# Optimization experiments

Measured on AMD Instinct MI355X. Metric: run time of the kernel, lower is better.

## Reference

```python
import jax, jax.numpy as jnp
import numpy as np

D_MODEL = 768
N_HEADS = 12
D_K = D_MODEL // N_HEADS
BATCH = 1
SEQ = 4096


def setup_inputs() -> dict:
    key = jax.random.key(0)
    kx, kq, kk, kv, ko = jax.random.split(key, 5)
    s = 1.0 / np.sqrt(D_MODEL)
    return {
        "x": jax.random.normal(kx, (BATCH, SEQ, D_MODEL), dtype=jnp.float32),
        "wq": jax.random.normal(kq, (D_MODEL, D_MODEL), dtype=jnp.float32) * s,
        "wk": jax.random.normal(kk, (D_MODEL, D_MODEL), dtype=jnp.float32) * s,
        "wv": jax.random.normal(kv, (D_MODEL, D_MODEL), dtype=jnp.float32) * s,
        "wo": jax.random.normal(ko, (D_MODEL, D_MODEL), dtype=jnp.float32) * s,
    }


def reference(x, wq, wk, wv, wo):
    B, S, D = x.shape
    H, dk = N_HEADS, D_K
    # nn.Linear(x) = x @ W.T ; reshape to [B,H,S,dk]
    def proj(w):
        return (x @ w.T).reshape(B, S, H, dk).transpose(0, 2, 1, 3)
    q, k, v = proj(wq), proj(wk), proj(wv)
    scores = jnp.einsum('bhqd,bhkd->bhqk', q, k) / np.sqrt(dk).astype(np.float32)
    attn = jax.nn.softmax(scores, axis=-1)
    out = jnp.einsum('bhqk,bhkd->bhqd', attn, v)
    out = out.transpose(0, 2, 1, 3).reshape(B, S, D)
    return out @ wo.T
```

## Files before the change

### kernel.cpp

```cpp
#include <hip/hip_runtime.h>
#include <stdint.h>

#define SEQ 4096
#define DMODEL 768
#define NHEADS 12
#define DKH 64

typedef __attribute__((ext_vector_type(8))) short short8;
typedef __attribute__((ext_vector_type(4))) float floatx4;
typedef __attribute__((ext_vector_type(16))) float floatx16;

__device__ __forceinline__ unsigned short f2bf(float f) {
    unsigned int u = __float_as_uint(f);
    u += 0x7fffu + ((u >> 16) & 1u);
    return (unsigned short)(u >> 16);
}

__device__ __forceinline__ float exp2fast(float x) {
    return __builtin_amdgcn_exp2f(x);
}

__device__ __forceinline__ unsigned int cvt_pk_bf16(float lo, float hi) {
    unsigned int r;
    asm("v_cvt_pk_bf16_f32 %0, %1, %2" : "=v"(r) : "v"(lo), "v"(hi));
    return r;
}

__device__ __forceinline__ int swz(int row, int colb) {
    return colb ^ ((row & 7) << 4);
}

__device__ __forceinline__ void async_copy16(void* lds, const void* g) {
    __builtin_amdgcn_global_load_lds(
        (const __attribute__((address_space(1))) void*)g,
        (__attribute__((address_space(3))) void*)lds,
        16, 0, 0);
}

__global__ __launch_bounds__(256) void castk(const float* __restrict__ src,
                                             unsigned short* __restrict__ dst,
                                             int n4) {
    int i = blockIdx.x * 256 + threadIdx.x;
    if (i >= n4) return;
    float4 v = ((const float4*)src)[i];
    ushort4 o;
    o.x = f2bf(v.x); o.y = f2bf(v.y); o.z = f2bf(v.z); o.w = f2bf(v.w);
    ((ushort4*)dst)[i] = o;
}

__global__ __launch_bounds__(256) void castw(const float* __restrict__ w0,
                                             const float* __restrict__ w1,
                                             const float* __restrict__ w2,
                                             const float* __restrict__ w3,
                                             unsigned short* __restrict__ dst) {
    int b = blockIdx.x;
    int wsel = b / 576;
    int i = (b % 576) * 256 + threadIdx.x;
    const float* src = (wsel == 0) ? w0 : (wsel == 1) ? w1 : (wsel == 2) ? w2 : w3;
    float4 v = ((const float4*)src)[i];
    ushort4 o;
    o.x = f2bf(v.x); o.y = f2bf(v.y); o.z = f2bf(v.z); o.w = f2bf(v.w);
    ((ushort4*)(dst + (size_t)wsel * 589824))[i] = o;
}

#define STAGE_G(bsel, kb)                                                              \
    do {                                                                               \
        char* As_ = smem + (bsel) * 24576;                                             \
        _Pragma("unroll") for (int ii = 0; ii < 4; ii++) {                             \
            int o = ii * 4096 + t * 16;                                                \
            int row = o >> 7, colb = o & 127;                                          \
            async_copy16(As_ + ii * 4096 + wid * 1024,                                 \
                         (const char*)A + ((size_t)(rowBase + row) * DMODEL + (kb)) * 2 \
                             + swz(row, colb));                                        \
        }                                                                              \
        _Pragma("unroll") for (int ii = 0; ii < 2; ii++) {                             \
            int o = ii * 4096 + t * 16;                                                \
            int row = o >> 7, colb = o & 127;                                          \
            async_copy16(As_ + 16384 + ii * 4096 + wid * 1024,                         \
                         (const char*)B + ((size_t)(colBase + row) * DMODEL + (kb)) * 2 \
                             + swz(row, colb));                                        \
        }                                                                              \
    } while (0)

#define GEMM_COMPUTE(As, Bs)                                                           \
    do {                                                                               \
        short8 a_[4][2], b_[2][2];                                                     \
        _Pragma("unroll") for (int m = 0; m < 4; m++)                                  \
            _Pragma("unroll") for (int kk = 0; kk < 2; kk++) {                         \
                int row = wr * 64 + m * 16 + lr;                                       \
                int colb = kk * 64 + lg * 16;                                          \
                a_[m][kk] = *(const short8*)((As) + row * 128 + swz(row, colb));       \
            }                                                                          \
        _Pragma("unroll") for (int n = 0; n < 2; n++)                                  \
            _Pragma("unroll") for (int kk = 0; kk < 2; kk++) {                         \
                int row = wc * 32 + n * 16 + lr;                                       \
                int colb = kk * 64 + lg * 16;                                          \
                b_[n][kk] = *(const short8*)((Bs) + row * 128 + swz(row, colb));       \
            }                                                                          \
        _Pragma("unroll") for (int m = 0; m < 4; m++)                                  \
            _Pragma("unroll") for (int n = 0; n < 2; n++)                              \
                _Pragma("unroll") for (int kk = 0; kk < 2; kk++)                       \
                    acc[m][n] = __builtin_amdgcn_mfma_f32_16x16x32_bf16(               \
                        a_[m][kk], b_[n][kk], acc[m][n], 0, 0, 0);                     \
    } while (0)

__global__ __launch_bounds__(256, 2)
void gemm_qkv(const unsigned short* __restrict__ A,
              const unsigned short* __restrict__ W,
              unsigned short* __restrict__ OutBase, float qscale) {
    __shared__ __align__(128) char smem[49152];

    const int t = threadIdx.x;
    const int wid = t >> 6, lane = t & 63;
    const int lr = lane & 15, lg = lane >> 4;
    const int wr = wid >> 1, wc = wid & 1;
    const int rowBase = blockIdx.x * 128;
    const int proj = blockIdx.y / 12;
    const int colBase = (blockIdx.y % 12) * 64;
    const unsigned short* B = W + (size_t)proj * 589824;

    const floatx4 zero4 = {0.f, 0.f, 0.f, 0.f};
    floatx4 acc[4][2];
#pragma unroll
    for (int m = 0; m < 4; m++)
#pragma unroll
        for (int n = 0; n < 2; n++) acc[m][n] = zero4;

    STAGE_G(0, 0);
    for (int i = 0; i < 12; ++i) {
        __builtin_amdgcn_s_barrier();
        __builtin_amdgcn_sched_barrier(0);
        if (i < 11) {
            STAGE_G((i + 1) & 1, (i + 1) * 64);
            asm volatile("s_waitcnt vmcnt(6)" ::: "memory");
        } else {
            asm volatile("s_waitcnt vmcnt(0)" ::: "memory");
        }
        __builtin_amdgcn_s_barrier();
        __builtin_amdgcn_sched_barrier(0);
        char* As = smem + (i & 1) * 24576;
        GEMM_COMPUTE(As, As + 16384);
    }

    if (proj < 2) {
        unsigned short* O = OutBase + (size_t)proj * 3145728;
        float scale = (proj == 0) ? qscale : 1.0f;
#pragma unroll
        for (int m = 0; m < 4; m++)
#pragma unroll
            for (int n = 0; n < 2; n++)
#pragma unroll
                for (int r = 0; r < 4; r++) {
                    int srow = rowBase + wr * 64 + m * 16 + lg * 4 + r;
                    int col = colBase + wc * 32 + n * 16 + lr;
                    int h = col >> 6, d = col & 63;
                    O[((size_t)h * SEQ + srow) * DKH + d] = f2bf(acc[m][n][r] * scale);
                }
    } else {
        unsigned short* O = OutBase + 6291456;
#pragma unroll
        for (int m = 0; m < 4; m++)
#pragma unroll
            for (int n = 0; n < 2; n++) {
                int srow0 = rowBase + wr * 64 + m * 16 + lg * 4;
                int pos0 = (srow0 & ~15) | ((srow0 & 4) << 1) | ((srow0 & 8) >> 1);
                int col = colBase + wc * 32 + n * 16 + lr;
                ushort4 o4;
                o4.x = f2bf(acc[m][n][0]);
                o4.y = f2bf(acc[m][n][1]);
                o4.z = f2bf(acc[m][n][2]);
                o4.w = f2bf(acc[m][n][3]);
                *(ushort4*)(O + (size_t)col * SEQ + pos0) = o4;
            }
    }
}

__global__ __launch_bounds__(256, 2)
void gemm_o(const unsigned short* __restrict__ A,
            const unsigned short* __restrict__ B,
            float* __restrict__ Out) {
    __shared__ __align__(128) char smem[49152];

    const int t = threadIdx.x;
    const int wid = t >> 6, lane = t & 63;
    const int lr = lane & 15, lg = lane >> 4;
    const int wr = wid >> 1, wc = wid & 1;
    const int rowBase = blockIdx.x * 128;
    const int colBase = blockIdx.y * 64;

    const floatx4 zero4 = {0.f, 0.f, 0.f, 0.f};
    floatx4 acc[4][2];
#pragma unroll
    for (int m = 0; m < 4; m++)
#pragma unroll
        for (int n = 0; n < 2; n++) acc[m][n] = zero4;

    STAGE_G(0, 0);
    for (int i = 0; i < 12; ++i) {
        __builtin_amdgcn_s_barrier();
        __builtin_amdgcn_sched_barrier(0);
        if (i < 11) {
            STAGE_G((i + 1) & 1, (i + 1) * 64);
            asm volatile("s_waitcnt vmcnt(6)" ::: "memory");
        } else {
            asm volatile("s_waitcnt vmcnt(0)" ::: "memory");
        }
        __builtin_amdgcn_s_barrier();
        __builtin_amdgcn_sched_barrier(0);
        char* As = smem + (i & 1) * 24576;
        GEMM_COMPUTE(As, As + 16384);
    }

#pragma unroll
    for (int m = 0; m < 4; m++)
#pragma unroll
        for (int n = 0; n < 2; n++)
#pragma unroll
            for (int r = 0; r < 4; r++) {
                int srow = rowBase + wr * 64 + m * 16 + lg * 4 + r;
                int col = colBase + wc * 32 + n * 16 + lr;
                Out[(size_t)srow * DMODEL + col] = acc[m][n][r];
            }
}

#define STAGE_K8(bsel, kv0)                                                            \
    do {                                                                               \
        char* Kd_ = smem + (bsel) * 16384;                                             \
        _Pragma("unroll") for (int ii = 0; ii < 4; ii++) {                             \
            int cc = ii * 256 + wid * 64 + lane;                                       \
            int gk = cc >> 6, qd = (cc >> 1) & 31, hh = cc & 1;                        \
            int kb2 = gk >> 2, ks2 = gk & 3;                                           \
            int key = kb2 * 32 + qd;                                                   \
            async_copy16(Kd_ + (ii * 256 + wid * 64) * 16,                             \
                         (const char*)(Kp + headOff) + (size_t)((kv0) + key) * 128     \
                             + (ks2 * 2 + hh) * 16);                                   \
        }                                                                              \
    } while (0)

#define STAGE_V8(kv0)                                                                  \
    do {                                                                               \
        char* Vd_ = smem + 32768;                                                      \
        _Pragma("unroll") for (int ii = 0; ii < 4; ii++) {                             \
            int cc = ii * 256 + wid * 64 + lane;                                       \
            int gv = cc >> 6, qd = (cc >> 1) & 31, hh = cc & 1;                        \
            int fbv = gv & 1, cv = (gv >> 1) & 3, ev = gv >> 3;                        \
            int feat = fbv * 32 + qd;                                                  \
            int p0 = ev * 64 + cv * 16 + hh * 8;                                       \
            async_copy16(Vd_ + (ii * 256 + wid * 64) * 16,                             \
                         (const char*)Vt                                               \
                             + ((size_t)(h * DKH + feat) * SEQ + (kv0) + p0) * 2);     \
        }                                                                              \
    } while (0)

__global__ __launch_bounds__(256, 2)
void attn_k(const unsigned short* __restrict__ Q,
            const unsigned short* __restrict__ Kp,
            const unsigned short* __restrict__ Vt,
            unsigned short* __restrict__ AO) {
    __shared__ __align__(128) char smem[49152];

    const int t = threadIdx.x;
    const int wid = t >> 6, lane = t & 63;
    const int q31 = lane & 31, hi = lane >> 5;
    const int g = wid >> 1, e = wid & 1;

    int nid = (blockIdx.x & 7) * 48 + (blockIdx.x >> 3);
    const int h = nid >> 5, qb = nid & 31;
    const size_t headOff = (size_t)h * SEQ * DKH;

    short8 qf0[4], qf1[4];
    {
        const unsigned short* qp0 =
            Q + headOff + (size_t)(qb * 128 + g * 64 + q31) * DKH + hi * 8;
        const unsigned short* qp1 = qp0 + 32 * DKH;
#pragma unroll
        for (int ks = 0; ks < 4; ks++) {
            qf0[ks] = *(const short8*)(qp0 + ks * 16);
            qf1[ks] = *(const short8*)(qp1 + ks * 16);
        }
    }

    const floatx16 z16 = {0.f, 0.f, 0.f, 0.f, 0.f, 0.f, 0.f, 0.f,
                          0.f, 0.f, 0.f, 0.f, 0.f, 0.f, 0.f, 0.f};
    float mrun[2] = {-3.0e38f, -3.0e38f}, lrun[2] = {0.f, 0.f};
    floatx16 accO[2][2] = {{z16, z16}, {z16, z16}};

    STAGE_K8(0, 0);

    for (int tt = 0; tt < 32; ++tt) {
        asm volatile("s_waitcnt vmcnt(0)" ::: "memory");
        __builtin_amdgcn_s_barrier();
        __builtin_amdgcn_sched_barrier(0);
        STAGE_V8(tt * 128);
        if (tt < 31) STAGE_K8((tt + 1) & 1, (tt + 1) * 128);
        __builtin_amdgcn_sched_barrier(0);

        const char* Ks = smem + (tt & 1) * 16384;
        const char* Vs = smem + 32768;

        floatx16 s[2][2] = {{z16, z16}, {z16, z16}};
        __builtin_amdgcn_s_setprio(1);
#pragma unroll
        for (int kb = 0; kb < 2; kb++) {
            const int kb2 = e * 2 + kb;
#pragma unroll
            for (int ks = 0; ks < 4; ks++) {
                short8 kf = *(const short8*)(
                    Ks + ((kb2 * 4 + ks) * 64 + q31 * 2 + hi) * 16);
                s[0][kb] = __builtin_amdgcn_mfma_f32_32x32x16_bf16(kf, qf0[ks], s[0][kb], 0, 0, 0);
                s[1][kb] = __builtin_amdgcn_mfma_f32_32x32x16_bf16(kf, qf1[ks], s[1][kb], 0, 0, 0);
            }
        }
        __builtin_amdgcn_s_setprio(0);

#pragma unroll
        for (int u = 0; u < 2; u++) {
            float mk[2];
#pragma unroll
            for (int kb = 0; kb < 2; kb++) {
                float a = fmaxf(fmaxf(s[u][kb][0], s[u][kb][1]), fmaxf(s[u][kb][2], s[u][kb][3]));
                float b = fmaxf(fmaxf(s[u][kb][4], s[u][kb][5]), fmaxf(s[u][kb][6], s[u][kb][7]));
                float c = fmaxf(fmaxf(s[u][kb][8], s[u][kb][9]), fmaxf(s[u][kb][10], s[u][kb][11]));
                float d = fmaxf(fmaxf(s[u][kb][12], s[u][kb][13]), fmaxf(s[u][kb][14], s[u][kb][15]));
                mk[kb] = fmaxf(fmaxf(a, b), fmaxf(c, d));
            }
            float mt = fmaxf(mk[0], mk[1]);
            mt = fmaxf(mt, __shfl_xor(mt, 32));
            if (!__all(mt <= mrun[u] + 8.0f)) {
                float mnew = fmaxf(mrun[u], mt);
                float al = exp2fast(mrun[u] - mnew);
#pragma unroll
                for (int fb = 0; fb < 2; fb++)
#pragma unroll
                    for (int j = 0; j < 16; j++) accO[u][fb][j] *= al;
                lrun[u] *= al;
                mrun[u] = mnew;
            }
#pragma unroll
            for (int kb = 0; kb < 2; kb++)
#pragma unroll
                for (int j = 0; j < 16; j++) s[u][kb][j] = exp2fast(s[u][kb][j] - mrun[u]);
            float sum = 0.f;
#pragma unroll
            for (int kb = 0; kb < 2; kb++) {
                float a = (s[u][kb][0] + s[u][kb][1]) + (s[u][kb][2] + s[u][kb][3]);
                float b = (s[u][kb][4] + s[u][kb][5]) + (s[u][kb][6] + s[u][kb][7]);
                float c = (s[u][kb][8] + s[u][kb][9]) + (s[u][kb][10] + s[u][kb][11]);
                float d = (s[u][kb][12] + s[u][kb][13]) + (s[u][kb][14] + s[u][kb][15]);
                sum += (a + b) + (c + d);
            }
            sum += __shfl_xor(sum, 32);
            lrun[u] += sum;
        }

        if (tt < 31) asm volatile("s_waitcnt vmcnt(4)" ::: "memory");
        else         asm volatile("s_waitcnt vmcnt(0)" ::: "memory");
        __builtin_amdgcn_s_barrier();
        __builtin_amdgcn_sched_barrier(0);

        __builtin_amdgcn_s_setprio(1);
#pragma unroll
        for (int c = 0; c < 4; c++) {
            const int kb = c >> 1, r0 = (c & 1) * 8;
            uint4 pw0, pw1;
            pw0.x = cvt_pk_bf16(s[0][kb][r0 + 0], s[0][kb][r0 + 1]);
            pw0.y = cvt_pk_bf16(s[0][kb][r0 + 2], s[0][kb][r0 + 3]);
            pw0.z = cvt_pk_bf16(s[0][kb][r0 + 4], s[0][kb][r0 + 5]);
            pw0.w = cvt_pk_bf16(s[0][kb][r0 + 6], s[0][kb][r0 + 7]);
            pw1.x = cvt_pk_bf16(s[1][kb][r0 + 0], s[1][kb][r0 + 1]);
            pw1.y = cvt_pk_bf16(s[1][kb][r0 + 2], s[1][kb][r0 + 3]);
            pw1.z = cvt_pk_bf16(s[1][kb][r0 + 4], s[1][kb][r0 + 5]);
            pw1.w = cvt_pk_bf16(s[1][kb][r0 + 6], s[1][kb][r0 + 7]);
            short8 pf0 = *(const short8*)&pw0;
            short8 pf1 = *(const short8*)&pw1;
#pragma unroll
            for (int fb = 0; fb < 2; fb++) {
                short8 vf = *(const short8*)(
                    Vs + (((e * 4 + c) * 2 + fb) * 64 + q31 * 2 + hi) * 16);
                accO[0][fb] = __builtin_amdgcn_mfma_f32_32x32x16_bf16(vf, pf0, accO[0][fb], 0, 0, 0);
                accO[1][fb] = __builtin_amdgcn_mfma_f32_32x32x16_bf16(vf, pf1, accO[1][fb], 0, 0, 0);
            }
        }
        __builtin_amdgcn_s_setprio(0);
    }

    __builtin_amdgcn_s_barrier();
    if (e == 1) {
#pragma unroll
        for (int u = 0; u < 2; u++) {
            char* R = smem + (((g * 2 + u) * 64) + lane) * 144;
#pragma unroll
            for (int fb = 0; fb < 2; fb++)
#pragma unroll
                for (int j4 = 0; j4 < 4; j4++) {
                    floatx4 v4 = {accO[u][fb][j4 * 4 + 0], accO[u][fb][j4 * 4 + 1],
                                  accO[u][fb][j4 * 4 + 2], accO[u][fb][j4 * 4 + 3]};
                    *(floatx4*)(R + fb * 64 + j4 * 16) = v4;
                }
            *(float*)(R + 128) = mrun[u];
            *(float*)(R + 132) = lrun[u];
        }
        asm volatile("s_waitcnt lgkmcnt(0)" ::: "memory");
    }
    __builtin_amdgcn_s_barrier();
    __builtin_amdgcn_sched_barrier(0);
    if (e == 0) {
#pragma unroll
        for (int u = 0; u < 2; u++) {
            const char* R = smem + (((g * 2 + u) * 64) + lane) * 144;
            float m1 = *(const float*)(R + 128);
            float l1 = *(const float*)(R + 132);
            float m = fmaxf(mrun[u], m1);
            float a0 = exp2fast(mrun[u] - m), a1 = exp2fast(m1 - m);
            float inv = 1.0f / (lrun[u] * a0 + l1 * a1);
            int srow = qb * 128 + g * 64 + u * 32 + q31;
#pragma unroll
            for (int fb = 0; fb < 2; fb++)
#pragma unroll
                for (int rq = 0; rq < 4; rq++) {
                    floatx4 p4 = *(const floatx4*)(R + fb * 64 + rq * 16);
                    ushort4 o4;
                    o4.x = f2bf((accO[u][fb][4 * rq + 0] * a0 + p4[0] * a1) * inv);
                    o4.y = f2bf((accO[u][fb][4 * rq + 1] * a0 + p4[1] * a1) * inv);
                    o4.z = f2bf((accO[u][fb][4 * rq + 2] * a0 + p4[2] * a1) * inv);
                    o4.w = f2bf((accO[u][fb][4 * rq + 3] * a0 + p4[3] * a1) * inv);
                    int col = h * DKH + fb * 32 + rq * 8 + hi * 4;
                    *(ushort4*)(AO + (size_t)srow * DMODEL + col) = o4;
                }
        }
    }
}

extern "C" void kernel_launch(void* const* d_in, const int* in_sizes, int n_in,
                              void* d_out, int out_size, void* d_ws, size_t ws_size,
                              hipStream_t stream) {
    const float* x  = (const float*)d_in[0];
    const float* wq = (const float*)d_in[1];
    const float* wk = (const float*)d_in[2];
    const float* wv = (const float*)d_in[3];
    const float* wo = (const float*)d_in[4];

    char* ws = (char*)d_ws;
    unsigned short* xb  = (unsigned short*)(ws + 0);
    unsigned short* wqb = (unsigned short*)(ws + 6291456);
    unsigned short* wob = (unsigned short*)(ws + 9830400);
    unsigned short* Qb  = (unsigned short*)(ws + 11010048);
    unsigned short* Kb  = (unsigned short*)(ws + 17301504);
    unsigned short* VTb = (unsigned short*)(ws + 23592960);
    unsigned short* AOb = (unsigned short*)(ws + 29884416);

    castk<<<3072, 256, 0, stream>>>(x, xb, 786432);
    castw<<<2304, 256, 0, stream>>>(wq, wk, wv, wo, wqb);

    gemm_qkv<<<dim3(32, 36), 256, 0, stream>>>(xb, wqb, Qb, 0.18033688f);

    attn_k<<<dim3(384), 256, 0, stream>>>(Qb, Kb, VTb, AOb);

    gemm_o<<<dim3(32, 12), 256, 0, stream>>>(AOb, wob, (float*)d_out);
}
```

Baseline: 127.8 us.

## Split attention KV across four waves per 64-query block, doubling grid

New measurement: 121.9 us. 4.6% less time.

```diff
diff --git a/kernel.cpp b/kernel.cpp
--- a/kernel.cpp
+++ b/kernel.cpp
@@ -223,36 +223,7 @@
             }
 }
 
-#define STAGE_K8(bsel, kv0)                                                            \
-    do {                                                                               \
-        char* Kd_ = smem + (bsel) * 16384;                                             \
-        _Pragma("unroll") for (int ii = 0; ii < 4; ii++) {                             \
-            int cc = ii * 256 + wid * 64 + lane;                                       \
-            int gk = cc >> 6, qd = (cc >> 1) & 31, hh = cc & 1;                        \
-            int kb2 = gk >> 2, ks2 = gk & 3;                                           \
-            int key = kb2 * 32 + qd;                                                   \
-            async_copy16(Kd_ + (ii * 256 + wid * 64) * 16,                             \
-                         (const char*)(Kp + headOff) + (size_t)((kv0) + key) * 128     \
-                             + (ks2 * 2 + hh) * 16);                                   \
-        }                                                                              \
-    } while (0)
-
-#define STAGE_V8(kv0)                                                                  \
-    do {                                                                               \
-        char* Vd_ = smem + 32768;                                                      \
-        _Pragma("unroll") for (int ii = 0; ii < 4; ii++) {                             \
-            int cc = ii * 256 + wid * 64 + lane;                                       \
-            int gv = cc >> 6, qd = (cc >> 1) & 31, hh = cc & 1;                        \
-            int fbv = gv & 1, cv = (gv >> 1) & 3, ev = gv >> 3;                        \
-            int feat = fbv * 32 + qd;                                                  \
-            int p0 = ev * 64 + cv * 16 + hh * 8;                                       \
-            async_copy16(Vd_ + (ii * 256 + wid * 64) * 16,                             \
-                         (const char*)Vt                                               \
-                             + ((size_t)(h * DKH + feat) * SEQ + (kv0) + p0) * 2);     \
-        }                                                                              \
-    } while (0)
-
-__global__ __launch_bounds__(256, 2)
+__global__ __launch_bounds__(256, 3)
 void attn_k(const unsigned short* __restrict__ Q,
             const unsigned short* __restrict__ Kp,
             const unsigned short* __restrict__ Vt,
@@ -262,22 +233,38 @@
     const int t = threadIdx.x;
     const int wid = t >> 6, lane = t & 63;
     const int q31 = lane & 31, hi = lane >> 5;
-    const int g = wid >> 1, e = wid & 1;
-
-    int nid = (blockIdx.x & 7) * 48 + (blockIdx.x >> 3);
-    const int h = nid >> 5, qb = nid & 31;
+    const int e = wid;
+    const int slot16 = (q31 * 2 + hi) * 16;
+
+    int nid = (blockIdx.x & 7) * 96 + (blockIdx.x >> 3);
+    const int h = nid >> 6, qb = nid & 63;
     const size_t headOff = (size_t)h * SEQ * DKH;
 
     short8 qf0[4], qf1[4];
     {
         const unsigned short* qp0 =
-            Q + headOff + (size_t)(qb * 128 + g * 64 + q31) * DKH + hi * 8;
+            Q + headOff + (size_t)(qb * 64 + q31) * DKH + hi * 8;
         const unsigned short* qp1 = qp0 + 32 * DKH;
 #pragma unroll
         for (int ks = 0; ks < 4; ks++) {
             qf0[ks] = *(const short8*)(qp0 + ks * 16);
             qf1[ks] = *(const short8*)(qp1 + ks * 16);
         }
+    }
+
+    const char* ksrc[4];
+    const char* vsrc[4];
+#pragma unroll
+    for (int ii = 0; ii < 4; ii++) {
+        int cc = ii * 256 + wid * 64 + lane;
+        int gk = cc >> 6, qd = (cc >> 1) & 31, hh = cc & 1;
+        int kb2 = gk >> 2, ks2 = gk & 3;
+        ksrc[ii] = (const char*)(Kp + headOff) + (size_t)(kb2 * 32 + qd) * 128
+                   + (ks2 * 2 + hh) * 16;
+        int fbv = gk & 1, cv = (gk >> 1) & 3, ev = gk >> 3;
+        vsrc[ii] = (const char*)Vt
+                   + ((size_t)(h * DKH + fbv * 32 + qd) * SEQ
+                      + ev * 64 + cv * 16 + hh * 8) * 2;
     }
 
     const floatx16 z16 = {0.f, 0.f, 0.f, 0.f, 0.f, 0.f, 0.f, 0.f,
@@ -285,46 +272,55 @@
     float mrun[2] = {-3.0e38f, -3.0e38f}, lrun[2] = {0.f, 0.f};
     floatx16 accO[2][2] = {{z16, z16}, {z16, z16}};
 
-    STAGE_K8(0, 0);
+#pragma unroll
+    for (int ii = 0; ii < 4; ii++) {
+        async_copy16(smem + (ii * 256 + wid * 64) * 16, ksrc[ii]);
+        ksrc[ii] += 16384;
+    }
 
     for (int tt = 0; tt < 32; ++tt) {
         asm volatile("s_waitcnt vmcnt(0)" ::: "memory");
         __builtin_amdgcn_s_barrier();
         __builtin_amdgcn_sched_barrier(0);
-        STAGE_V8(tt * 128);
-        if (tt < 31) STAGE_K8((tt + 1) & 1, (tt + 1) * 128);
+        {
+            char* Vd = smem + 32768;
+#pragma unroll
+            for (int ii = 0; ii < 4; ii++) {
+                async_copy16(Vd + (ii * 256 + wid * 64) * 16, vsrc[ii]);
+                vsrc[ii] += 256;
+            }
+        }
+        if (tt < 31) {
+            char* Kd = smem + ((tt + 1) & 1) * 16384;
+#pragma unroll
+            for (int ii = 0; ii < 4; ii++) {
+                async_copy16(Kd + (ii * 256 + wid * 64) * 16, ksrc[ii]);
+                ksrc[ii] += 16384;
+            }
+        }
         __builtin_amdgcn_sched_barrier(0);
 
         const char* Ks = smem + (tt & 1) * 16384;
         const char* Vs = smem + 32768;
 
-        floatx16 s[2][2] = {{z16, z16}, {z16, z16}};
+        floatx16 s0 = z16, s1 = z16;
         __builtin_amdgcn_s_setprio(1);
 #pragma unroll
-        for (int kb = 0; kb < 2; kb++) {
-            const int kb2 = e * 2 + kb;
-#pragma unroll
-            for (int ks = 0; ks < 4; ks++) {
-                short8 kf = *(const short8*)(
-                    Ks + ((kb2 * 4 + ks) * 64 + q31 * 2 + hi) * 16);
-                s[0][kb] = __builtin_amdgcn_mfma_f32_32x32x16_bf16(kf, qf0[ks], s[0][kb], 0, 0, 0);
-                s[1][kb] = __builtin_amdgcn_mfma_f32_32x32x16_bf16(kf, qf1[ks], s[1][kb], 0, 0, 0);
-            }
+        for (int ks = 0; ks < 4; ks++) {
+            short8 kf = *(const short8*)(Ks + (e * 4 + ks) * 1024 + slot16);
+            s0 = __builtin_amdgcn_mfma_f32_32x32x16_bf16(kf, qf0[ks], s0, 0, 0, 0);
+            s1 = __builtin_amdgcn_mfma_f32_32x32x16_bf16(kf, qf1[ks], s1, 0, 0, 0);
         }
         __builtin_amdgcn_s_setprio(0);
 
 #pragma unroll
         for (int u = 0; u < 2; u++) {
-            float mk[2];
-#pragma unroll
-            for (int kb = 0; kb < 2; kb++) {
-                float a = fmaxf(fmaxf(s[u][kb][0], s[u][kb][1]), fmaxf(s[u][kb][2], s[u][kb][3]));
-                float b = fmaxf(fmaxf(s[u][kb][4], s[u][kb][5]), fmaxf(s[u][kb][6], s[u][kb][7]));
-                float c = fmaxf(fmaxf(s[u][kb][8], s[u][kb][9]), fmaxf(s[u][kb][10], s[u][kb][11]));
-                float d = fmaxf(fmaxf(s[u][kb][12], s[u][kb][13]), fmaxf(s[u][kb][14], s[u][kb][15]));
-                mk[kb] = fmaxf(fmaxf(a, b), fmaxf(c, d));
-            }
-            float mt = fmaxf(mk[0], mk[1]);
+            floatx16& s = (u == 0) ? s0 : s1;
+            float a = fmaxf(fmaxf(s[0], s[1]), fmaxf(s[2], s[3]));
+            float b = fmaxf(fmaxf(s[4], s[5]), fmaxf(s[6], s[7]));
+            float c = fmaxf(fmaxf(s[8], s[9]), fmaxf(s[10], s[11]));
+            float d = fmaxf(fmaxf(s[12], s[13]), fmaxf(s[14], s[15]));
+            float mt = fmaxf(fmaxf(a, b), fmaxf(c, d));
             mt = fmaxf(mt, __shfl_xor(mt, 32));
             if (!__all(mt <= mrun[u] + 8.0f)) {
                 float mnew = fmaxf(mrun[u], mt);
@@ -337,18 +333,12 @@
                 mrun[u] = mnew;
             }
 #pragma unroll
-            for (int kb = 0; kb < 2; kb++)
-#pragma unroll
-                for (int j = 0; j < 16; j++) s[u][kb][j] = exp2fast(s[u][kb][j] - mrun[u]);
-            float sum = 0.f;
-#pragma unroll
-            for (int kb = 0; kb < 2; kb++) {
-                float a = (s[u][kb][0] + s[u][kb][1]) + (s[u][kb][2] + s[u][kb][3]);
-                float b = (s[u][kb][4] + s[u][kb][5]) + (s[u][kb][6] + s[u][kb][7]);
-                float c = (s[u][kb][8] + s[u][kb][9]) + (s[u][kb][10] + s[u][kb][11]);
-                float d = (s[u][kb][12] + s[u][kb][13]) + (s[u][kb][14] + s[u][kb][15]);
-                sum += (a + b) + (c + d);
-            }
+            for (int j = 0; j < 16; j++) s[j] = exp2fast(s[j] - mrun[u]);
+            float sa = (s[0] + s[1]) + (s[2] + s[3]);
+            float sb = (s[4] + s[5]) + (s[6] + s[7]);
+            float sc = (s[8] + s[9]) + (s[10] + s[11]);
+            float sd = (s[12] + s[13]) + (s[14] + s[15]);
+            float sum = (sa + sb) + (sc + sd);
             sum += __shfl_xor(sum, 32);
             lrun[u] += sum;
         }
@@ -360,23 +350,23 @@
 
         __builtin_amdgcn_s_setprio(1);
 #pragma unroll
-        for (int c = 0; c < 4; c++) {
-            const int kb = c >> 1, r0 = (c & 1) * 8;
+        for (int cp = 0; cp < 2; cp++) {
+            const int r0 = cp * 8;
             uint4 pw0, pw1;
-            pw0.x = cvt_pk_bf16(s[0][kb][r0 + 0], s[0][kb][r0 + 1]);
-            pw0.y = cvt_pk_bf16(s[0][kb][r0 + 2], s[0][kb][r0 + 3]);
-            pw0.z = cvt_pk_bf16(s[0][kb][r0 + 4], s[0][kb][r0 + 5]);
-            pw0.w = cvt_pk_bf16(s[0][kb][r0 + 6], s[0][kb][r0 + 7]);
-            pw1.x = cvt_pk_bf16(s[1][kb][r0 + 0], s[1][kb][r0 + 1]);
-            pw1.y = cvt_pk_bf16(s[1][kb][r0 + 2], s[1][kb][r0 + 3]);
-            pw1.z = cvt_pk_bf16(s[1][kb][r0 + 4], s[1][kb][r0 + 5]);
-            pw1.w = cvt_pk_bf16(s[1][kb][r0 + 6], s[1][kb][r0 + 7]);
+            pw0.x = cvt_pk_bf16(s0[r0 + 0], s0[r0 + 1]);
+            pw0.y = cvt_pk_bf16(s0[r0 + 2], s0[r0 + 3]);
+            pw0.z = cvt_pk_bf16(s0[r0 + 4], s0[r0 + 5]);
+            pw0.w = cvt_pk_bf16(s0[r0 + 6], s0[r0 + 7]);
+            pw1.x = cvt_pk_bf16(s1[r0 + 0], s1[r0 + 1]);
+            pw1.y = cvt_pk_bf16(s1[r0 + 2], s1[r0 + 3]);
+            pw1.z = cvt_pk_bf16(s1[r0 + 4], s1[r0 + 5]);
+            pw1.w = cvt_pk_bf16(s1[r0 + 6], s1[r0 + 7]);
             short8 pf0 = *(const short8*)&pw0;
             short8 pf1 = *(const short8*)&pw1;
 #pragma unroll
             for (int fb = 0; fb < 2; fb++) {
-                short8 vf = *(const short8*)(
-                    Vs + (((e * 4 + c) * 2 + fb) * 64 + q31 * 2 + hi) * 16);
+                int chunk = ((e >> 1) * 4 + (e & 1) * 2 + cp) * 2 + fb;
+                short8 vf = *(const short8*)(Vs + chunk * 1024 + slot16);
                 accO[0][fb] = __builtin_amdgcn_mfma_f32_32x32x16_bf16(vf, pf0, accO[0][fb], 0, 0, 0);
                 accO[1][fb] = __builtin_amdgcn_mfma_f32_32x32x16_bf16(vf, pf1, accO[1][fb], 0, 0, 0);
             }
@@ -385,10 +375,11 @@
     }
 
     __builtin_amdgcn_s_barrier();
-    if (e == 1) {
+#define MSLOT(w, u) (smem + (((w) * 2 + (u)) * 64 + lane) * 160)
+    if (e & 1) {
 #pragma unroll
         for (int u = 0; u < 2; u++) {
-            char* R = smem + (((g * 2 + u) * 64) + lane) * 144;
+            char* R = MSLOT(e >> 1, u);
 #pragma unroll
             for (int fb = 0; fb < 2; fb++)
 #pragma unroll
@@ -403,17 +394,57 @@
         asm volatile("s_waitcnt lgkmcnt(0)" ::: "memory");
     }
     __builtin_amdgcn_s_barrier();
-    __builtin_amdgcn_sched_barrier(0);
+    if (!(e & 1)) {
+#pragma unroll
+        for (int u = 0; u < 2; u++) {
+            const char* R = MSLOT(e >> 1, u);
+            float m1 = *(const float*)(R + 128);
+            float l1 = *(const float*)(R + 132);
+            float m = fmaxf(mrun[u], m1);
+            float a0 = exp2fast(mrun[u] - m), a1 = exp2fast(m1 - m);
+#pragma unroll
+            for (int fb = 0; fb < 2; fb++)
+#pragma unroll
+                for (int j4 = 0; j4 < 4; j4++) {
+                    floatx4 p4 = *(const floatx4*)(R + fb * 64 + j4 * 16);
+#pragma unroll
+                    for (int j = 0; j < 4; j++)
+                        accO[u][fb][j4 * 4 + j] = accO[u][fb][j4 * 4 + j] * a0 + p4[j] * a1;
+                }
+            lrun[u] = lrun[u] * a0 + l1 * a1;
+            mrun[u] = m;
+        }
+    }
+    asm volatile("s_waitcnt lgkmcnt(0)" ::: "memory");
+    __builtin_amdgcn_s_barrier();
+    if (e == 2) {
+#pragma unroll
+        for (int u = 0; u < 2; u++) {
+            char* R = MSLOT(0, u);
+#pragma unroll
+            for (int fb = 0; fb < 2; fb++)
+#pragma unroll
+                for (int j4 = 0; j4 < 4; j4++) {
+                    floatx4 v4 = {accO[u][fb][j4 * 4 + 0], accO[u][fb][j4 * 4 + 1],
+                                  accO[u][fb][j4 * 4 + 2], accO[u][fb][j4 * 4 + 3]};
+                    *(floatx4*)(R + fb * 64 + j4 * 16) = v4;
+                }
+            *(float*)(R + 128) = mrun[u];
+            *(float*)(R + 132) = lrun[u];
+        }
+        asm volatile("s_waitcnt lgkmcnt(0)" ::: "memory");
+    }
+    __builtin_amdgcn_s_barrier();
     if (e == 0) {
 #pragma unroll
         for (int u = 0; u < 2; u++) {
-            const char* R = smem + (((g * 2 + u) * 64) + lane) * 144;
+            const char* R = MSLOT(0, u);
             float m1 = *(const float*)(R + 128);
             float l1 = *(const float*)(R + 132);
             float m = fmaxf(mrun[u], m1);
             float a0 = exp2fast(mrun[u] - m), a1 = exp2fast(m1 - m);
             float inv = 1.0f / (lrun[u] * a0 + l1 * a1);
-            int srow = qb * 128 + g * 64 + u * 32 + q31;
+            int srow = qb * 64 + u * 32 + q31;
 #pragma unroll
             for (int fb = 0; fb < 2; fb++)
 #pragma unroll
@@ -429,6 +460,7 @@
                 }
         }
     }
+#undef MSLOT
 }
 
 extern "C" void kernel_launch(void* const* d_in, const int* in_sizes, int n_in,
@@ -454,7 +486,7 @@
 
     gemm_qkv<<<dim3(32, 36), 256, 0, stream>>>(xb, wqb, Qb, 0.18033688f);
 
-    attn_k<<<dim3(384), 256, 0, stream>>>(Qb, Kb, VTb, AOb);
+    attn_k<<<dim3(768), 256, 0, stream>>>(Qb, Kb, VTb, AOb);
 
     gemm_o<<<dim3(32, 12), 256, 0, stream>>>(AOb, wob, (float*)d_out);
 }
```
